# Kernel tuning notes

Measured on AMD Instinct MI355X. Metric: run time of the kernel, lower is better.

## Reference

```python
import jax, jax.numpy as jnp
import numpy as np

NUM_NODES = 50000
NUM_EDGES = 800000
IN_CH = 128
HID = 128
NUM_LAYERS = 3
CONF_HID = 64
TAU0 = 1.0


def _glorot(key, shape):
    lim = (6.0 / (shape[0] + shape[1])) ** 0.5
    return jax.random.uniform(key, shape, jnp.float32, -lim, lim)


def setup_inputs() -> dict:
    key = jax.random.key(0)
    ks = jax.random.split(key, 16)
    inp = {
        "x": jax.random.normal(ks[0], (NUM_NODES, IN_CH), jnp.float32),
        "edge_index": jax.random.randint(ks[1], (2, NUM_EDGES), 0, NUM_NODES, jnp.int32),
    }
    dims = [(IN_CH, HID)] + [(HID, HID)] * (NUM_LAYERS - 1)
    for i, (di, do) in enumerate(dims):
        inp[f"conv_w{i}"] = _glorot(ks[2 + i], (di, do))
        inp[f"conv_b{i}"] = jnp.zeros((do,), jnp.float32)
    inp["conf_w1"] = _glorot(ks[8], (HID, CONF_HID))
    inp["conf_b1"] = jnp.zeros((CONF_HID,), jnp.float32)
    inp["conf_w2"] = _glorot(ks[9], (CONF_HID, 2))
    inp["conf_b2"] = jnp.zeros((2,), jnp.float32)
    inp["temp_w"] = _glorot(ks[10], (HID, 1))
    return inp


def _gcn_conv(x, W, b, src, dst):
    # PyG GCNConv: linear -> add self loops -> sym-normalized aggregate -> bias
    h = x @ W
    loop = jnp.arange(NUM_NODES, dtype=src.dtype)
    s = jnp.concatenate([src, loop])
    d = jnp.concatenate([dst, loop])
    deg = jax.ops.segment_sum(jnp.ones(d.shape, h.dtype), d, num_segments=NUM_NODES)
    dinv = jnp.where(deg > 0, deg ** -0.5, 0.0)
    norm = dinv[s] * dinv[d]  # [E+N]
    out = jax.ops.segment_sum(h[s] * norm[:, None], d, num_segments=NUM_NODES)
    return out + b


def _forward(x, edge_index, conv_ws, conv_bs, conf_w1, conf_b1, conf_w2, conf_b2, temp_w):
    src, dst = edge_index[0], edge_index[1]
    gkey = jax.random.key(42)
    z = jnp.zeros((NUM_NODES, HID), jnp.float32)
    continue_mask = jnp.ones((NUM_NODES,), bool)
    exit_layers = jnp.full((NUM_NODES,), NUM_LAYERS, jnp.int32)
    active = []
    for layer_idx in range(NUM_LAYERS):
        x = _gcn_conv(x, conv_ws[layer_idx], conv_bs[layer_idx], src, dst)
        if layer_idx < NUM_LAYERS - 1:
            x = jax.nn.gelu(x, approximate=False)  # eval mode: dropout is identity
        active.append(jnp.sum(continue_mask).astype(jnp.int32))
        logits = jax.nn.relu(x @ conf_w1 + conf_b1) @ conf_w2 + conf_b2  # [N,2]
        temp = 1.0 / (jax.nn.softplus(x @ temp_w) + TAU0)  # [N,1], always finite
        u = jax.random.uniform(jax.random.fold_in(gkey, layer_idx), logits.shape,
                               jnp.float32, 1e-10, 1.0)
        gumbels = -jnp.log(-jnp.log(u))
        y = jax.nn.softmax((logits + gumbels) / temp, axis=-1)
        exit_decision = y[:, 1] > y[:, 0]
        newly_exited = exit_decision & continue_mask
        z = z + x * newly_exited[:, None].astype(x.dtype)
        exit_layers = jnp.where(newly_exited, layer_idx, exit_layers)
        continue_mask = continue_mask & ~exit_decision
    z = z + x * continue_mask[:, None].astype(x.dtype)
    return z, exit_layers, jnp.stack(active)


def reference(x, edge_index, conv_w0, conv_b0, conv_w1, conv_b1, conv_w2, conv_b2,
              conf_w1, conf_b1, conf_w2, conf_b2, temp_w):
    return _forward(x, edge_index,
                    [conv_w0, conv_w1, conv_w2], [conv_b0, conv_b1, conv_b2],
                    conf_w1, conf_b1, conf_w2, conf_b2, temp_w)
```

## Files before the change

### kernel.cpp

```cpp
#include <hip/hip_runtime.h>
#include <stdint.h>

#define NN 50000
#define NE 800000
#define CH 128

typedef double d4 __attribute__((ext_vector_type(4)));

__host__ __device__ inline void tf2x32(uint32_t k0, uint32_t k1, uint32_t& x0, uint32_t& x1) {
  uint32_t ks2 = k0 ^ k1 ^ 0x1BD11BDAu;
  x0 += k0; x1 += k1;
#define ROTL(v, r) (((v) << (r)) | ((v) >> (32 - (r))))
#define RND(r) { x0 += x1; x1 = ROTL(x1, r); x1 ^= x0; }
  RND(13) RND(15) RND(26) RND(6)
  x0 += k1; x1 += ks2 + 1u;
  RND(17) RND(29) RND(16) RND(24)
  x0 += ks2; x1 += k0 + 2u;
  RND(13) RND(15) RND(26) RND(6)
  x0 += k0; x1 += k1 + 3u;
  RND(17) RND(29) RND(16) RND(24)
  x0 += k1; x1 += ks2 + 4u;
  RND(13) RND(15) RND(26) RND(6)
  x0 += ks2; x1 += k0 + 5u;
#undef RND
#undef ROTL
}

__device__ inline float bits_to_u(uint32_t b) {
  float f = __uint_as_float(0x3F800000u | (b >> 9)) - 1.0f;
  f = f + 1e-10f;
  return fmaxf(1e-10f, f);
}

__global__ __launch_bounds__(256) void deg_k(const int* __restrict__ dst, int* __restrict__ degi) {
  int i = blockIdx.x * 256 + threadIdx.x;
  if (i < NE) atomicAdd(&degi[dst[i]], 1);
}

__global__ __launch_bounds__(256) void dinv_k(const int* __restrict__ degi, float* __restrict__ dinv) {
  int n = blockIdx.x * 256 + threadIdx.x;
  if (n < NN) {
    float d = (float)(degi[n] + 1);
    dinv[n] = 1.0f / sqrtf(d);
  }
}

__global__ __launch_bounds__(256) void scan1_k(const int* __restrict__ degi, int* __restrict__ offs,
                                               int* __restrict__ part) {
  __shared__ int tmp[256];
  int t = threadIdx.x, b = blockIdx.x, i = b * 256 + t;
  int v = (i < NN) ? degi[i] : 0;
  tmp[t] = v;
  __syncthreads();
  for (int s = 1; s < 256; s <<= 1) {
    int a = (t >= s) ? tmp[t - s] : 0;
    __syncthreads();
    tmp[t] += a;
    __syncthreads();
  }
  int incl = tmp[t];
  if (i < NN) offs[i] = incl - v;
  if (t == 255) part[b] = incl;
}

__global__ void scan2_k(int* part, int nparts) {
  if (threadIdx.x == 0 && blockIdx.x == 0) {
    int run = 0;
    for (int i = 0; i < nparts; ++i) { int v = part[i]; part[i] = run; run += v; }
  }
}

__global__ __launch_bounds__(256) void scan3_k(int* __restrict__ offs, const int* __restrict__ part) {
  int i = blockIdx.x * 256 + threadIdx.x;
  if (i < NN) offs[i] += part[blockIdx.x];
  if (i == 0) offs[NN] = NE;
}

__global__ __launch_bounds__(256) void place_k(const int* __restrict__ dst, const int* __restrict__ offs,
                                               int* __restrict__ cnt, int* __restrict__ eids) {
  int i = blockIdx.x * 256 + threadIdx.x;
  if (i < NE) {
    int d = dst[i];
    int p = offs[d] + atomicAdd(&cnt[d], 1);
    eids[p] = i;
  }
}

__global__ __launch_bounds__(256) void sort_k(const int* __restrict__ offs, int* __restrict__ eids) {
  int n = blockIdx.x * 256 + threadIdx.x;
  if (n >= NN) return;
  int s0 = offs[n], s1 = offs[n + 1];
  for (int i = s0 + 1; i < s1; ++i) {
    int v = eids[i];
    int j = i - 1;
    while (j >= s0 && eids[j] > v) { eids[j + 1] = eids[j]; --j; }
    eids[j + 1] = v;
  }
}

__global__ __launch_bounds__(256) void gath_k(const int* __restrict__ eids, const int* __restrict__ src,
                                              const int* __restrict__ dst, const float* __restrict__ dinv,
                                              int* __restrict__ srcs, float* __restrict__ norms) {
  int p = blockIdx.x * 256 + threadIdx.x;
  if (p < NE) {
    int e = eids[p];
    int s = src[e];
    float nm = dinv[s] * dinv[dst[e]];
    srcs[p] = s;
    norms[p] = nm;
  }
}

__global__ __launch_bounds__(256) void gum_k(float* __restrict__ gum,
                                             uint32_t k00, uint32_t k01, uint32_t k10, uint32_t k11,
                                             uint32_t k20, uint32_t k21) {
  int i = blockIdx.x * 256 + threadIdx.x;
  if (i >= 3 * NN) return;
  int l = i / NN;
  int n = i - l * NN;
  uint32_t kx, ky;
  if (l == 0) { kx = k00; ky = k01; }
  else if (l == 1) { kx = k10; ky = k11; }
  else { kx = k20; ky = k21; }
  int j0 = 2 * n, j1 = 2 * n + 1;
  uint32_t w0, w1;
  if (j0 < NN) {
    uint32_t a0 = (uint32_t)j0, a1 = (uint32_t)(j0 + NN);
    tf2x32(kx, ky, a0, a1); w0 = a0;
    uint32_t b0 = (uint32_t)j1, b1 = (uint32_t)(j1 + NN);
    tf2x32(kx, ky, b0, b1); w1 = b0;
  } else {
    uint32_t a0 = (uint32_t)(j0 - NN), a1 = (uint32_t)j0;
    tf2x32(kx, ky, a0, a1); w0 = a1;
    uint32_t b0 = (uint32_t)(j1 - NN), b1 = (uint32_t)j1;
    tf2x32(kx, ky, b0, b1); w1 = b1;
  }
  float u0 = bits_to_u(w0), u1 = bits_to_u(w1);
  gum[2 * (size_t)i]     = -logf(-logf(u0));
  gum[2 * (size_t)i + 1] = -logf(-logf(u1));
}

__global__ __launch_bounds__(256) void einit_k(float* __restrict__ eout) {
  int i = blockIdx.x * 256 + threadIdx.x;
  if (i < NN) eout[i] = 3.0f;
}

__global__ __launch_bounds__(256) void lin_k(const float* __restrict__ x, const float* __restrict__ W,
                                             float* __restrict__ h) {
  __shared__ float Ws[32 * 128];
  __shared__ float xs[64][36];
  int t = threadIdx.x;
  int row0 = blockIdx.x << 6;
  int tr = t & 15, tc = t >> 4;
  float4 acc[4][2];
#pragma unroll
  for (int i = 0; i < 4; ++i) { acc[i][0] = make_float4(0,0,0,0); acc[i][1] = make_float4(0,0,0,0); }

  for (int kt = 0; kt < 4; ++kt) {
    __syncthreads();
    {
      const float4* W4 = (const float4*)(W + (size_t)(kt * 32) * 128);
      float4* Ws4 = (float4*)Ws;
#pragma unroll
      for (int i = 0; i < 4; ++i) Ws4[t + 256 * i] = W4[t + 256 * i];
    }
    {
#pragma unroll
      for (int i = 0; i < 2; ++i) {
        int f = t + 256 * i;
        int row = f >> 3, c4 = f & 7;
        int gr = row0 + row;
        float4 v = make_float4(0,0,0,0);
        if (gr < NN) v = ((const float4*)x)[(size_t)gr * 32 + kt * 8 + c4];
        *(float4*)&xs[row][4 * c4] = v;
      }
    }
    __syncthreads();
    const float4* Ws4 = (const float4*)Ws;
#pragma unroll
    for (int kk = 0; kk < 32; kk += 4) {
      float4 xv[4];
#pragma unroll
      for (int i = 0; i < 4; ++i) xv[i] = *(const float4*)&xs[tr + 16 * i][kk];
#pragma unroll
      for (int d = 0; d < 4; ++d) {
        float4 w0 = Ws4[(kk + d) * 32 + tc];
        float4 w1 = Ws4[(kk + d) * 32 + 16 + tc];
#pragma unroll
        for (int i = 0; i < 4; ++i) {
          float xd = ((const float*)&xv[i])[d];
          acc[i][0].x += xd * w0.x; acc[i][0].y += xd * w0.y;
          acc[i][0].z += xd * w0.z; acc[i][0].w += xd * w0.w;
          acc[i][1].x += xd * w1.x; acc[i][1].y += xd * w1.y;
          acc[i][1].z += xd * w1.z; acc[i][1].w += xd * w1.w;
        }
      }
    }
  }
#pragma unroll
  for (int i = 0; i < 4; ++i) {
    int gr = row0 + tr + 16 * i;
    if (gr < NN) {
      ((float4*)h)[(size_t)gr * 32 + tc] = acc[i][0];
      ((float4*)h)[(size_t)gr * 32 + 16 + tc] = acc[i][1];
    }
  }
}

__device__ inline float gelu_exact(float v) {
  return 0.5f * v * (1.0f + erff(v / 1.4142135623730951f));
}

__global__ __launch_bounds__(256) void agg_k(const float* __restrict__ h, const float* __restrict__ dinv,
                                             const int* __restrict__ offs, const int* __restrict__ srcs,
                                             const float* __restrict__ norms, const float* __restrict__ bias,
                                             float* __restrict__ xout, int act) {
  int lane = threadIdx.x & 63, w = threadIdx.x >> 6;
  int n = blockIdx.x * 4 + w;
  if (n >= NN) return;
  int s0 = offs[n], s1 = offs[n + 1];
  double a0 = 0.0, a1 = 0.0;
  for (int p0 = s0; p0 < s1; p0 += 64) {
    int m = s1 - p0; if (m > 64) m = 64;
    int sv = 0; float nv = 0.f;
    if (lane < m) {
      sv = __builtin_nontemporal_load(&srcs[p0 + lane]);
      nv = __builtin_nontemporal_load(&norms[p0 + lane]);
    }
    int i = 0;
    for (; i + 8 <= m; i += 8) {
      int   sA = __shfl(sv, i),     sB = __shfl(sv, i + 1), sC = __shfl(sv, i + 2), sD = __shfl(sv, i + 3);
      int   sE = __shfl(sv, i + 4), sF = __shfl(sv, i + 5), sG = __shfl(sv, i + 6), sH = __shfl(sv, i + 7);
      float nA = __shfl(nv, i),     nB = __shfl(nv, i + 1), nC = __shfl(nv, i + 2), nD = __shfl(nv, i + 3);
      float nE = __shfl(nv, i + 4), nF = __shfl(nv, i + 5), nG = __shfl(nv, i + 6), nH = __shfl(nv, i + 7);
      float2 hA = *(const float2*)&h[(size_t)sA * CH + 2 * lane];
      float2 hB = *(const float2*)&h[(size_t)sB * CH + 2 * lane];
      float2 hC = *(const float2*)&h[(size_t)sC * CH + 2 * lane];
      float2 hD = *(const float2*)&h[(size_t)sD * CH + 2 * lane];
      float2 hE = *(const float2*)&h[(size_t)sE * CH + 2 * lane];
      float2 hF = *(const float2*)&h[(size_t)sF * CH + 2 * lane];
      float2 hG = *(const float2*)&h[(size_t)sG * CH + 2 * lane];
      float2 hH = *(const float2*)&h[(size_t)sH * CH + 2 * lane];
      a0 += (double)(hA.x * nA); a1 += (double)(hA.y * nA);
      a0 += (double)(hB.x * nB); a1 += (double)(hB.y * nB);
      a0 += (double)(hC.x * nC); a1 += (double)(hC.y * nC);
      a0 += (double)(hD.x * nD); a1 += (double)(hD.y * nD);
      a0 += (double)(hE.x * nE); a1 += (double)(hE.y * nE);
      a0 += (double)(hF.x * nF); a1 += (double)(hF.y * nF);
      a0 += (double)(hG.x * nG); a1 += (double)(hG.y * nG);
      a0 += (double)(hH.x * nH); a1 += (double)(hH.y * nH);
    }
    for (; i + 4 <= m; i += 4) {
      int   sA = __shfl(sv, i),     sB = __shfl(sv, i + 1), sC = __shfl(sv, i + 2), sD = __shfl(sv, i + 3);
      float nA = __shfl(nv, i),     nB = __shfl(nv, i + 1), nC = __shfl(nv, i + 2), nD = __shfl(nv, i + 3);
      float2 hA = *(const float2*)&h[(size_t)sA * CH + 2 * lane];
      float2 hB = *(const float2*)&h[(size_t)sB * CH + 2 * lane];
      float2 hC = *(const float2*)&h[(size_t)sC * CH + 2 * lane];
      float2 hD = *(const float2*)&h[(size_t)sD * CH + 2 * lane];
      a0 += (double)(hA.x * nA); a1 += (double)(hA.y * nA);
      a0 += (double)(hB.x * nB); a1 += (double)(hB.y * nB);
      a0 += (double)(hC.x * nC); a1 += (double)(hC.y * nC);
      a0 += (double)(hD.x * nD); a1 += (double)(hD.y * nD);
    }
    for (; i < m; ++i) {
      int   s = __shfl(sv, i);
      float nm = __shfl(nv, i);
      float2 hv = *(const float2*)&h[(size_t)s * CH + 2 * lane];
      a0 += (double)(hv.x * nm); a1 += (double)(hv.y * nm);
    }
  }
  float dv = dinv[n];
  float selfn = dv * dv;
  float2 hn = *(const float2*)&h[(size_t)n * CH + 2 * lane];
  a0 += (double)(hn.x * selfn); a1 += (double)(hn.y * selfn);
  float r0 = (float)a0 + bias[2 * lane];
  float r1 = (float)a1 + bias[2 * lane + 1];
  if (act) { r0 = gelu_exact(r0); r1 = gelu_exact(r1); }
  float2 o; o.x = r0; o.y = r1;
  *(float2*)&xout[(size_t)n * CH + 2 * lane] = o;
}

template <int MODE>
__global__ __launch_bounds__(256) void decide_k(const float* __restrict__ x, const float* __restrict__ W1,
                                                const float* __restrict__ b1, const float* __restrict__ W2,
                                                const float* __restrict__ b2, const float* __restrict__ gum,
                                                float* __restrict__ zout, float* __restrict__ eout,
                                                float layerf) {
  __shared__ float b1s[64];
  __shared__ float w2s[128];
  __shared__ float b2s[2];
  __shared__ float xs[4][16][132];
  int t = threadIdx.x;
  if (t < 64) b1s[t] = b1[t];
  if (t < 128) w2s[t] = W2[t];
  if (t < 2) b2s[t] = b2[t];

  int lane = t & 63, w = t >> 6;
  int n0 = blockIdx.x * 64 + w * 16;
#pragma unroll
  for (int i = 0; i < 8; ++i) {
    int f = lane + 64 * i;
    int row = f >> 5, c4 = f & 31;
    int gr = n0 + row;
    float4 v = make_float4(0.f, 0.f, 0.f, 0.f);
    if (gr < NN) v = ((const float4*)x)[(size_t)gr * 32 + c4];
    *(float4*)&xs[w][row][4 * c4] = v;
  }

  int g = lane >> 4, r = lane & 15;
  bool writer = (r < 4);
  int mynode = n0 + 4 * g + r;
  float ev = 3.0f;
  float gg0 = 0.f, gg1 = 0.f;
  if (writer && mynode < NN) {
    if (MODE > 0) ev = eout[mynode];
    gg0 = gum[2 * (size_t)mynode];
    gg1 = gum[2 * (size_t)mynode + 1];
  }
  bool m_act = writer && (mynode < NN) && (MODE == 0 || ev == 3.0f);
  unsigned long long actmask = __ballot(m_act);
  __syncthreads();
  if (MODE > 0 && actmask == 0ULL) return;

  d4 acc0 = {0., 0., 0., 0.}, acc1 = {0., 0., 0., 0.};
  d4 acc2 = {0., 0., 0., 0.}, acc3 = {0., 0., 0., 0.};
#pragma unroll 4
  for (int ks = 0; ks < 32; ++ks) {
    int k = 4 * ks + g;
    double av = (double)xs[w][r][k];
    const float* Wk = W1 + (size_t)k * 64;
    double b0 = (double)Wk[r];
    double b1v = (double)Wk[16 + r];
    double b2v = (double)Wk[32 + r];
    double b3v = (double)Wk[48 + r];
    acc0 = __builtin_amdgcn_mfma_f64_16x16x4f64(av, b0, acc0, 0, 0, 0);
    acc1 = __builtin_amdgcn_mfma_f64_16x16x4f64(av, b1v, acc1, 0, 0, 0);
    acc2 = __builtin_amdgcn_mfma_f64_16x16x4f64(av, b2v, acc2, 0, 0, 0);
    acc3 = __builtin_amdgcn_mfma_f64_16x16x4f64(av, b3v, acc3, 0, 0, 0);
  }

  double p0[4], p1[4];
#pragma unroll
  for (int i = 0; i < 4; ++i) {
    float h0 = fmaxf((float)acc0[i] + b1s[r], 0.f);
    float h1 = fmaxf((float)acc1[i] + b1s[16 + r], 0.f);
    float h2 = fmaxf((float)acc2[i] + b1s[32 + r], 0.f);
    float h3 = fmaxf((float)acc3[i] + b1s[48 + r], 0.f);
    double q0 = (double)h0 * (double)w2s[2 * r] + (double)h1 * (double)w2s[2 * (16 + r)] +
                (double)h2 * (double)w2s[2 * (32 + r)] + (double)h3 * (double)w2s[2 * (48 + r)];
    double q1 = (double)h0 * (double)w2s[2 * r + 1] + (double)h1 * (double)w2s[2 * (16 + r) + 1] +
                (double)h2 * (double)w2s[2 * (32 + r) + 1] + (double)h3 * (double)w2s[2 * (48 + r) + 1];
#pragma unroll
    for (int off = 1; off <= 8; off <<= 1) {
      q0 += __shfl_xor(q0, off);
      q1 += __shfl_xor(q1, off);
    }
    p0[i] = q0; p1[i] = q1;
  }

  double q0sel = p0[0], q1sel = p1[0];
  if (r == 1) { q0sel = p0[1]; q1sel = p1[1]; }
  if (r == 2) { q0sel = p0[2]; q1sel = p1[2]; }
  if (r == 3) { q0sel = p0[3]; q1sel = p1[3]; }
  bool myex = false;
  if (writer && mynode < NN) {
    float l0 = (float)q0sel + b2s[0];
    float l1 = (float)q1sel + b2s[1];
    myex = (l1 + gg1) > (l0 + gg0);
  }
  unsigned long long exmask = __ballot(myex);

  if (m_act && myex) eout[mynode] = layerf;

#pragma unroll
  for (int i = 0; i < 16; ++i) {
    int bitpos = 16 * (i >> 2) + (i & 3);
    bool a = (actmask >> bitpos) & 1ULL;
    bool ee = (exmask >> bitpos) & 1ULL;
    if (a && (MODE == 2 || ee)) {
      int node = n0 + i;
      float2 v;
      v.x = xs[w][i][2 * lane];
      v.y = xs[w][i][2 * lane + 1];
      *(float2*)&zout[(size_t)node * CH + 2 * lane] = v;
    }
  }
}

__global__ __launch_bounds__(1024) void cnt_k(const float* __restrict__ eout, float* __restrict__ aout) {
  __shared__ int s1[16], s2[16];
  int t = threadIdx.x;
  int c1 = 0, c2 = 0;
  for (int i = t; i < NN; i += 1024) {
    float v = eout[i];
    c1 += (v < 0.5f);
    c2 += (v < 1.5f);
  }
#pragma unroll
  for (int off = 32; off >= 1; off >>= 1) { c1 += __shfl_xor(c1, off); c2 += __shfl_xor(c2, off); }
  if ((t & 63) == 0) { s1[t >> 6] = c1; s2[t >> 6] = c2; }
  __syncthreads();
  if (t == 0) {
    int a1 = 0, a2 = 0;
#pragma unroll
    for (int i = 0; i < 16; ++i) { a1 += s1[i]; a2 += s2[i]; }
    aout[0] = 50000.0f;
    aout[1] = (float)(NN - a1);
    aout[2] = (float)(NN - a2);
  }
}

extern "C" void kernel_launch(void* const* d_in, const int* in_sizes, int n_in,
                              void* d_out, int out_size, void* d_ws, size_t ws_size,
                              hipStream_t stream) {
  const float* x_in = (const float*)d_in[0];
  const int* eidx = (const int*)d_in[1];
  const int* esrc = eidx;
  const int* edst = eidx + NE;
  const float* convw[3] = {(const float*)d_in[2], (const float*)d_in[4], (const float*)d_in[6]};
  const float* convb[3] = {(const float*)d_in[3], (const float*)d_in[5], (const float*)d_in[7]};
  const float* cw1 = (const float*)d_in[8];
  const float* cb1 = (const float*)d_in[9];
  const float* cw2 = (const float*)d_in[10];
  const float* cb2 = (const float*)d_in[11];

  float* out = (float*)d_out;
  float* zout = out;
  float* eout = out + (size_t)NN * CH;
  float* aout = eout + NN;

  char* w = (char*)d_ws;
  float* P = (float*)w;   w += (size_t)NN * CH * 4;
  float* Q = (float*)w;   w += (size_t)NN * CH * 4;
  int* eids = (int*)w;    w += (size_t)NE * 4;
  float* norms = (float*)w; w += (size_t)NE * 4;
  float* gum = (float*)w; w += (size_t)3 * NN * 2 * 4;
  int* offs = (int*)w;    w += (size_t)(NN + 1) * 4;
  float* dinv = (float*)w; w += (size_t)NN * 4;
  char* zr0 = w;
  int* degi = (int*)w;    w += (size_t)NN * 4;
  int* cnt = (int*)w;     w += (size_t)NN * 4;
  int* parts = (int*)w;   w += 1024;

  hipMemsetAsync(zr0, 0, (size_t)(2 * NN) * 4, stream);

  uint32_t key[3][2];
  for (int l = 0; l < 3; ++l) {
    uint32_t a = 0u, b = (uint32_t)l;
    tf2x32(0u, 42u, a, b);
    key[l][0] = a; key[l][1] = b;
  }

  const int nblkN = (NN + 255) / 256;
  deg_k<<<(NE + 255) / 256, 256, 0, stream>>>(edst, degi);
  dinv_k<<<nblkN, 256, 0, stream>>>(degi, dinv);
  scan1_k<<<nblkN, 256, 0, stream>>>(degi, offs, parts);
  scan2_k<<<1, 64, 0, stream>>>(parts, nblkN);
  scan3_k<<<nblkN, 256, 0, stream>>>(offs, parts);
  place_k<<<(NE + 255) / 256, 256, 0, stream>>>(edst, offs, cnt, eids);
  sort_k<<<nblkN, 256, 0, stream>>>(offs, eids);
  gath_k<<<(NE + 255) / 256, 256, 0, stream>>>(eids, esrc, edst, dinv, eids, norms);
  gum_k<<<(3 * NN + 255) / 256, 256, 0, stream>>>(gum, key[0][0], key[0][1], key[1][0], key[1][1],
                                                  key[2][0], key[2][1]);
  einit_k<<<nblkN, 256, 0, stream>>>(eout);

  const int LB = (NN + 63) / 64;
  const int AB = (NN + 3) / 4;
  const int DB = (NN + 63) / 64;
  for (int l = 0; l < 3; ++l) {
    const float* xin = (l == 0) ? x_in : Q;
    lin_k<<<LB, 256, 0, stream>>>(xin, convw[l], P);
    agg_k<<<AB, 256, 0, stream>>>(P, dinv, offs, eids, norms, convb[l], Q, (l < 2) ? 1 : 0);
    if (l == 0)
      decide_k<0><<<DB, 256, 0, stream>>>(Q, cw1, cb1, cw2, cb2, gum, zout, eout, 0.0f);
    else if (l == 1)
      decide_k<1><<<DB, 256, 0, stream>>>(Q, cw1, cb1, cw2, cb2, gum + (size_t)NN * 2, zout, eout, 1.0f);
    else
      decide_k<2><<<DB, 256, 0, stream>>>(Q, cw1, cb1, cw2, cb2, gum + (size_t)2 * NN * 2, zout, eout, 2.0f);
  }
  cnt_k<<<1, 1024, 0, stream>>>(eout, aout);
}
```

Measured before the change: 526.9 us.

## Fuse exit-decision MLP into next layer's linear kernel and widen aggregation loads

```diff
diff --git a/kernel.cpp b/kernel.cpp
--- a/kernel.cpp
+++ b/kernel.cpp
@@ -37,16 +37,8 @@
   if (i < NE) atomicAdd(&degi[dst[i]], 1);
 }
 
-__global__ __launch_bounds__(256) void dinv_k(const int* __restrict__ degi, float* __restrict__ dinv) {
-  int n = blockIdx.x * 256 + threadIdx.x;
-  if (n < NN) {
-    float d = (float)(degi[n] + 1);
-    dinv[n] = 1.0f / sqrtf(d);
-  }
-}
-
 __global__ __launch_bounds__(256) void scan1_k(const int* __restrict__ degi, int* __restrict__ offs,
-                                               int* __restrict__ part) {
+                                               int* __restrict__ part, float* __restrict__ dinv) {
   __shared__ int tmp[256];
   int t = threadIdx.x, b = blockIdx.x, i = b * 256 + t;
   int v = (i < NN) ? degi[i] : 0;
@@ -59,7 +51,10 @@
     __syncthreads();
   }
   int incl = tmp[t];
-  if (i < NN) offs[i] = incl - v;
+  if (i < NN) {
+    offs[i] = incl - v;
+    dinv[i] = 1.0f / sqrtf((float)(v + 1));
+  }
   if (t == 255) part[b] = incl;
 }
 
@@ -140,18 +135,45 @@
   gum[2 * (size_t)i + 1] = -logf(-logf(u1));
 }
 
-__global__ __launch_bounds__(256) void einit_k(float* __restrict__ eout) {
-  int i = blockIdx.x * 256 + threadIdx.x;
-  if (i < NN) eout[i] = 3.0f;
-}
-
-__global__ __launch_bounds__(256) void lin_k(const float* __restrict__ x, const float* __restrict__ W,
-                                             float* __restrict__ h) {
+template <int DEC>
+__global__ __launch_bounds__(256) void lin_k(const float* __restrict__ xin, const float* __restrict__ W,
+                                             float* __restrict__ h, const float* __restrict__ W1,
+                                             const float* __restrict__ b1, const float* __restrict__ W2,
+                                             const float* __restrict__ b2, const float* __restrict__ gum,
+                                             float* __restrict__ zout, float* __restrict__ eout) {
   __shared__ float Ws[32 * 128];
   __shared__ float xs[64][36];
+  __shared__ float w2s[128];
+  __shared__ float b1s[64];
+  __shared__ float b2s[2];
   int t = threadIdx.x;
   int row0 = blockIdx.x << 6;
   int tr = t & 15, tc = t >> 4;
+
+  int lane = t & 63, w = t >> 6;
+  int g = lane >> 4, r = lane & 15;
+  int n0 = row0 + w * 16;
+  bool writer = (r < 4);
+  int mynode = n0 + 4 * g + r;
+  float ev = 3.0f, gg0 = 0.f, gg1 = 0.f;
+  unsigned long long actmask = 0ULL;
+  bool doMLP = false;
+  d4 acc0 = {0., 0., 0., 0.}, acc1 = {0., 0., 0., 0.};
+  d4 acc2 = {0., 0., 0., 0.}, acc3 = {0., 0., 0., 0.};
+  if (DEC >= 0) {
+    if (t < 64) b1s[t] = b1[t];
+    if (t < 128) w2s[t] = W2[t];
+    if (t < 2) b2s[t] = b2[t];
+    if (writer && mynode < NN) {
+      if (DEC == 1) ev = eout[mynode];
+      gg0 = gum[2 * (size_t)mynode];
+      gg1 = gum[2 * (size_t)mynode + 1];
+    }
+    bool m_act = writer && (mynode < NN) && (DEC == 0 || ev == 3.0f);
+    actmask = __ballot(m_act);
+    doMLP = (DEC == 0) || (actmask != 0ULL);
+  }
+
   float4 acc[4][2];
 #pragma unroll
   for (int i = 0; i < 4; ++i) { acc[i][0] = make_float4(0,0,0,0); acc[i][1] = make_float4(0,0,0,0); }
@@ -171,7 +193,7 @@
         int row = f >> 3, c4 = f & 7;
         int gr = row0 + row;
         float4 v = make_float4(0,0,0,0);
-        if (gr < NN) v = ((const float4*)x)[(size_t)gr * 32 + kt * 8 + c4];
+        if (gr < NN) v = ((const float4*)xin)[(size_t)gr * 32 + kt * 8 + c4];
         *(float4*)&xs[row][4 * c4] = v;
       }
     }
@@ -196,6 +218,23 @@
         }
       }
     }
+    if (DEC >= 0 && doMLP) {
+#pragma unroll
+      for (int ksl = 0; ksl < 8; ++ksl) {
+        int kl = 4 * ksl + g;
+        int kglob = kt * 32 + kl;
+        double av = (double)xs[w * 16 + r][kl];
+        const float* Wk = W1 + (size_t)kglob * 64;
+        double b0v = (double)Wk[r];
+        double b1v = (double)Wk[16 + r];
+        double b2v = (double)Wk[32 + r];
+        double b3v = (double)Wk[48 + r];
+        acc0 = __builtin_amdgcn_mfma_f64_16x16x4f64(av, b0v, acc0, 0, 0, 0);
+        acc1 = __builtin_amdgcn_mfma_f64_16x16x4f64(av, b1v, acc1, 0, 0, 0);
+        acc2 = __builtin_amdgcn_mfma_f64_16x16x4f64(av, b2v, acc2, 0, 0, 0);
+        acc3 = __builtin_amdgcn_mfma_f64_16x16x4f64(av, b3v, acc3, 0, 0, 0);
+      }
+    }
   }
 #pragma unroll
   for (int i = 0; i < 4; ++i) {
@@ -203,6 +242,55 @@
     if (gr < NN) {
       ((float4*)h)[(size_t)gr * 32 + tc] = acc[i][0];
       ((float4*)h)[(size_t)gr * 32 + 16 + tc] = acc[i][1];
+    }
+  }
+
+  if (DEC >= 0 && doMLP) {
+    double p0[4], p1[4];
+#pragma unroll
+    for (int i = 0; i < 4; ++i) {
+      float h0 = fmaxf((float)acc0[i] + b1s[r], 0.f);
+      float h1 = fmaxf((float)acc1[i] + b1s[16 + r], 0.f);
+      float h2 = fmaxf((float)acc2[i] + b1s[32 + r], 0.f);
+      float h3 = fmaxf((float)acc3[i] + b1s[48 + r], 0.f);
+      double q0 = (double)h0 * (double)w2s[2 * r] + (double)h1 * (double)w2s[2 * (16 + r)] +
+                  (double)h2 * (double)w2s[2 * (32 + r)] + (double)h3 * (double)w2s[2 * (48 + r)];
+      double q1 = (double)h0 * (double)w2s[2 * r + 1] + (double)h1 * (double)w2s[2 * (16 + r) + 1] +
+                  (double)h2 * (double)w2s[2 * (32 + r) + 1] + (double)h3 * (double)w2s[2 * (48 + r) + 1];
+#pragma unroll
+      for (int off = 1; off <= 8; off <<= 1) {
+        q0 += __shfl_xor(q0, off);
+        q1 += __shfl_xor(q1, off);
+      }
+      p0[i] = q0; p1[i] = q1;
+    }
+    double q0sel = p0[0], q1sel = p1[0];
+    if (r == 1) { q0sel = p0[1]; q1sel = p1[1]; }
+    if (r == 2) { q0sel = p0[2]; q1sel = p1[2]; }
+    if (r == 3) { q0sel = p0[3]; q1sel = p1[3]; }
+    bool myex = false;
+    if (writer && mynode < NN) {
+      float l0 = (float)q0sel + b2s[0];
+      float l1 = (float)q1sel + b2s[1];
+      myex = (l1 + gg1) > (l0 + gg0);
+    }
+    unsigned long long exmask = __ballot(myex);
+    bool m_act = (actmask >> (16 * g + r)) & 1ULL;
+    if (DEC == 0) {
+      if (writer && mynode < NN) eout[mynode] = myex ? 0.0f : 3.0f;
+    } else {
+      if (m_act && myex) eout[mynode] = 1.0f;
+    }
+#pragma unroll
+    for (int i = 0; i < 16; ++i) {
+      int bitpos = 16 * (i >> 2) + (i & 3);
+      bool a = (actmask >> bitpos) & 1ULL;
+      bool ee = (exmask >> bitpos) & 1ULL;
+      if (a && ee) {
+        int node = n0 + i;
+        float2 v = *(const float2*)&xin[(size_t)node * CH + 2 * lane];
+        *(float2*)&zout[(size_t)node * CH + 2 * lane] = v;
+      }
     }
   }
 }
@@ -218,8 +306,9 @@
   int lane = threadIdx.x & 63, w = threadIdx.x >> 6;
   int n = blockIdx.x * 4 + w;
   if (n >= NN) return;
+  int c4 = lane & 31, hh = lane >> 5;
   int s0 = offs[n], s1 = offs[n + 1];
-  double a0 = 0.0, a1 = 0.0;
+  double a0 = 0.0, a1 = 0.0, a2 = 0.0, a3 = 0.0;
   for (int p0 = s0; p0 < s1; p0 += 64) {
     int m = s1 - p0; if (m > 64) m = 64;
     int sv = 0; float nv = 0.f;
@@ -229,63 +318,49 @@
     }
     int i = 0;
     for (; i + 8 <= m; i += 8) {
-      int   sA = __shfl(sv, i),     sB = __shfl(sv, i + 1), sC = __shfl(sv, i + 2), sD = __shfl(sv, i + 3);
-      int   sE = __shfl(sv, i + 4), sF = __shfl(sv, i + 5), sG = __shfl(sv, i + 6), sH = __shfl(sv, i + 7);
-      float nA = __shfl(nv, i),     nB = __shfl(nv, i + 1), nC = __shfl(nv, i + 2), nD = __shfl(nv, i + 3);
-      float nE = __shfl(nv, i + 4), nF = __shfl(nv, i + 5), nG = __shfl(nv, i + 6), nH = __shfl(nv, i + 7);
-      float2 hA = *(const float2*)&h[(size_t)sA * CH + 2 * lane];
-      float2 hB = *(const float2*)&h[(size_t)sB * CH + 2 * lane];
-      float2 hC = *(const float2*)&h[(size_t)sC * CH + 2 * lane];
-      float2 hD = *(const float2*)&h[(size_t)sD * CH + 2 * lane];
-      float2 hE = *(const float2*)&h[(size_t)sE * CH + 2 * lane];
-      float2 hF = *(const float2*)&h[(size_t)sF * CH + 2 * lane];
-      float2 hG = *(const float2*)&h[(size_t)sG * CH + 2 * lane];
-      float2 hH = *(const float2*)&h[(size_t)sH * CH + 2 * lane];
-      a0 += (double)(hA.x * nA); a1 += (double)(hA.y * nA);
-      a0 += (double)(hB.x * nB); a1 += (double)(hB.y * nB);
-      a0 += (double)(hC.x * nC); a1 += (double)(hC.y * nC);
-      a0 += (double)(hD.x * nD); a1 += (double)(hD.y * nD);
-      a0 += (double)(hE.x * nE); a1 += (double)(hE.y * nE);
-      a0 += (double)(hF.x * nF); a1 += (double)(hF.y * nF);
-      a0 += (double)(hG.x * nG); a1 += (double)(hG.y * nG);
-      a0 += (double)(hH.x * nH); a1 += (double)(hH.y * nH);
-    }
-    for (; i + 4 <= m; i += 4) {
-      int   sA = __shfl(sv, i),     sB = __shfl(sv, i + 1), sC = __shfl(sv, i + 2), sD = __shfl(sv, i + 3);
-      float nA = __shfl(nv, i),     nB = __shfl(nv, i + 1), nC = __shfl(nv, i + 2), nD = __shfl(nv, i + 3);
-      float2 hA = *(const float2*)&h[(size_t)sA * CH + 2 * lane];
-      float2 hB = *(const float2*)&h[(size_t)sB * CH + 2 * lane];
-      float2 hC = *(const float2*)&h[(size_t)sC * CH + 2 * lane];
-      float2 hD = *(const float2*)&h[(size_t)sD * CH + 2 * lane];
-      a0 += (double)(hA.x * nA); a1 += (double)(hA.y * nA);
-      a0 += (double)(hB.x * nB); a1 += (double)(hB.y * nB);
-      a0 += (double)(hC.x * nC); a1 += (double)(hC.y * nC);
-      a0 += (double)(hD.x * nD); a1 += (double)(hD.y * nD);
-    }
-    for (; i < m; ++i) {
-      int   s = __shfl(sv, i);
-      float nm = __shfl(nv, i);
-      float2 hv = *(const float2*)&h[(size_t)s * CH + 2 * lane];
-      a0 += (double)(hv.x * nm); a1 += (double)(hv.y * nm);
-    }
-  }
-  float dv = dinv[n];
-  float selfn = dv * dv;
-  float2 hn = *(const float2*)&h[(size_t)n * CH + 2 * lane];
-  a0 += (double)(hn.x * selfn); a1 += (double)(hn.y * selfn);
-  float r0 = (float)a0 + bias[2 * lane];
-  float r1 = (float)a1 + bias[2 * lane + 1];
-  if (act) { r0 = gelu_exact(r0); r1 = gelu_exact(r1); }
-  float2 o; o.x = r0; o.y = r1;
-  *(float2*)&xout[(size_t)n * CH + 2 * lane] = o;
-}
-
-template <int MODE>
-__global__ __launch_bounds__(256) void decide_k(const float* __restrict__ x, const float* __restrict__ W1,
-                                                const float* __restrict__ b1, const float* __restrict__ W2,
-                                                const float* __restrict__ b2, const float* __restrict__ gum,
-                                                float* __restrict__ zout, float* __restrict__ eout,
-                                                float layerf) {
+      int   sA = __shfl(sv, i + hh),     sB = __shfl(sv, i + 2 + hh);
+      int   sC = __shfl(sv, i + 4 + hh), sD = __shfl(sv, i + 6 + hh);
+      float nA = __shfl(nv, i + hh),     nB = __shfl(nv, i + 2 + hh);
+      float nC = __shfl(nv, i + 4 + hh), nD = __shfl(nv, i + 6 + hh);
+      float4 hA = *(const float4*)&h[(size_t)sA * CH + 4 * c4];
+      float4 hB = *(const float4*)&h[(size_t)sB * CH + 4 * c4];
+      float4 hC = *(const float4*)&h[(size_t)sC * CH + 4 * c4];
+      float4 hD = *(const float4*)&h[(size_t)sD * CH + 4 * c4];
+      a0 += (double)(hA.x * nA); a1 += (double)(hA.y * nA); a2 += (double)(hA.z * nA); a3 += (double)(hA.w * nA);
+      a0 += (double)(hB.x * nB); a1 += (double)(hB.y * nB); a2 += (double)(hB.z * nB); a3 += (double)(hB.w * nB);
+      a0 += (double)(hC.x * nC); a1 += (double)(hC.y * nC); a2 += (double)(hC.z * nC); a3 += (double)(hC.w * nC);
+      a0 += (double)(hD.x * nD); a1 += (double)(hD.y * nD); a2 += (double)(hD.z * nD); a3 += (double)(hD.w * nD);
+    }
+    for (; i < m; i += 2) {
+      int   s = __shfl(sv, i + hh);
+      float nm = __shfl(nv, i + hh);
+      float4 hv = *(const float4*)&h[(size_t)s * CH + 4 * c4];
+      a0 += (double)(hv.x * nm); a1 += (double)(hv.y * nm); a2 += (double)(hv.z * nm); a3 += (double)(hv.w * nm);
+    }
+  }
+  a0 += __shfl_xor(a0, 32); a1 += __shfl_xor(a1, 32);
+  a2 += __shfl_xor(a2, 32); a3 += __shfl_xor(a3, 32);
+  if (hh == 0) {
+    float dv = dinv[n];
+    float selfn = dv * dv;
+    float4 hn = *(const float4*)&h[(size_t)n * CH + 4 * c4];
+    a0 += (double)(hn.x * selfn); a1 += (double)(hn.y * selfn);
+    a2 += (double)(hn.z * selfn); a3 += (double)(hn.w * selfn);
+    float4 bv = *(const float4*)&bias[4 * c4];
+    float r0 = (float)a0 + bv.x;
+    float r1 = (float)a1 + bv.y;
+    float r2 = (float)a2 + bv.z;
+    float r3 = (float)a3 + bv.w;
+    if (act) { r0 = gelu_exact(r0); r1 = gelu_exact(r1); r2 = gelu_exact(r2); r3 = gelu_exact(r3); }
+    float4 o; o.x = r0; o.y = r1; o.z = r2; o.w = r3;
+    *(float4*)&xout[(size_t)n * CH + 4 * c4] = o;
+  }
+}
+
+__global__ __launch_bounds__(256) void decide2_k(const float* __restrict__ x, const float* __restrict__ W1,
+                                                 const float* __restrict__ b1, const float* __restrict__ W2,
+                                                 const float* __restrict__ b2, const float* __restrict__ gum,
+                                                 float* __restrict__ zout, float* __restrict__ eout) {
   __shared__ float b1s[64];
   __shared__ float w2s[128];
   __shared__ float b2s[2];
@@ -310,17 +385,16 @@
   int g = lane >> 4, r = lane & 15;
   bool writer = (r < 4);
   int mynode = n0 + 4 * g + r;
-  float ev = 3.0f;
-  float gg0 = 0.f, gg1 = 0.f;
+  float ev = 3.0f, gg0 = 0.f, gg1 = 0.f;
   if (writer && mynode < NN) {
-    if (MODE > 0) ev = eout[mynode];
+    ev = eout[mynode];
     gg0 = gum[2 * (size_t)mynode];
     gg1 = gum[2 * (size_t)mynode + 1];
   }
-  bool m_act = writer && (mynode < NN) && (MODE == 0 || ev == 3.0f);
+  bool m_act = writer && (mynode < NN) && (ev == 3.0f);
   unsigned long long actmask = __ballot(m_act);
   __syncthreads();
-  if (MODE > 0 && actmask == 0ULL) return;
+  if (actmask == 0ULL) return;
 
   d4 acc0 = {0., 0., 0., 0.}, acc1 = {0., 0., 0., 0.};
   d4 acc2 = {0., 0., 0., 0.}, acc3 = {0., 0., 0., 0.};
@@ -370,14 +444,13 @@
   }
   unsigned long long exmask = __ballot(myex);
 
-  if (m_act && myex) eout[mynode] = layerf;
+  if (m_act && myex) eout[mynode] = 2.0f;
 
 #pragma unroll
   for (int i = 0; i < 16; ++i) {
     int bitpos = 16 * (i >> 2) + (i & 3);
     bool a = (actmask >> bitpos) & 1ULL;
-    bool ee = (exmask >> bitpos) & 1ULL;
-    if (a && (MODE == 2 || ee)) {
+    if (a) {
       int node = n0 + i;
       float2 v;
       v.x = xs[w][i][2 * lane];
@@ -391,10 +464,10 @@
   __shared__ int s1[16], s2[16];
   int t = threadIdx.x;
   int c1 = 0, c2 = 0;
-  for (int i = t; i < NN; i += 1024) {
-    float v = eout[i];
-    c1 += (v < 0.5f);
-    c2 += (v < 1.5f);
+  for (int i = t; i < NN / 4; i += 1024) {
+    float4 v = ((const float4*)eout)[i];
+    c1 += (v.x < 0.5f) + (v.y < 0.5f) + (v.z < 0.5f) + (v.w < 0.5f);
+    c2 += (v.x < 1.5f) + (v.y < 1.5f) + (v.z < 1.5f) + (v.w < 1.5f);
   }
 #pragma unroll
   for (int off = 32; off >= 1; off >>= 1) { c1 += __shfl_xor(c1, off); c2 += __shfl_xor(c2, off); }
@@ -453,8 +526,7 @@
 
   const int nblkN = (NN + 255) / 256;
   deg_k<<<(NE + 255) / 256, 256, 0, stream>>>(edst, degi);
-  dinv_k<<<nblkN, 256, 0, stream>>>(degi, dinv);
-  scan1_k<<<nblkN, 256, 0, stream>>>(degi, offs, parts);
+  scan1_k<<<nblkN, 256, 0, stream>>>(degi, offs, parts, dinv);
   scan2_k<<<1, 64, 0, stream>>>(parts, nblkN);
   scan3_k<<<nblkN, 256, 0, stream>>>(offs, parts);
   place_k<<<(NE + 255) / 256, 256, 0, stream>>>(edst, offs, cnt, eids);
@@ -462,21 +534,16 @@
   gath_k<<<(NE + 255) / 256, 256, 0, stream>>>(eids, esrc, edst, dinv, eids, norms);
   gum_k<<<(3 * NN + 255) / 256, 256, 0, stream>>>(gum, key[0][0], key[0][1], key[1][0], key[1][1],
                                                   key[2][0], key[2][1]);
-  einit_k<<<nblkN, 256, 0, stream>>>(eout);
 
   const int LB = (NN + 63) / 64;
   const int AB = (NN + 3) / 4;
-  const int DB = (NN + 63) / 64;
-  for (int l = 0; l < 3; ++l) {
-    const float* xin = (l == 0) ? x_in : Q;
-    lin_k<<<LB, 256, 0, stream>>>(xin, convw[l], P);
-    agg_k<<<AB, 256, 0, stream>>>(P, dinv, offs, eids, norms, convb[l], Q, (l < 2) ? 1 : 0);
-    if (l == 0)
-      decide_k<0><<<DB, 256, 0, stream>>>(Q, cw1, cb1, cw2, cb2, gum, zout, eout, 0.0f);
-    else if (l == 1)
-      decide_k<1><<<DB, 256, 0, stream>>>(Q, cw1, cb1, cw2, cb2, gum + (size_t)NN * 2, zout, eout, 1.0f);
-    else
-      decide_k<2><<<DB, 256, 0, stream>>>(Q, cw1, cb1, cw2, cb2, gum + (size_t)2 * NN * 2, zout, eout, 2.0f);
-  }
+  lin_k<-1><<<LB, 256, 0, stream>>>(x_in, convw[0], P, nullptr, nullptr, nullptr, nullptr,
+                                    nullptr, nullptr, nullptr);
+  agg_k<<<AB, 256, 0, stream>>>(P, dinv, offs, eids, norms, convb[0], Q, 1);
+  lin_k<0><<<LB, 256, 0, stream>>>(Q, convw[1], P, cw1, cb1, cw2, cb2, gum, zout, eout);
+  agg_k<<<AB, 256, 0, stream>>>(P, dinv, offs, eids, norms, convb[1], Q, 1);
+  lin_k<1><<<LB, 256, 0, stream>>>(Q, convw[2], P, cw1, cb1, cw2, cb2, gum + (size_t)NN * 2, zout, eout);
+  agg_k<<<AB, 256, 0, stream>>>(P, dinv, offs, eids, norms, convb[2], Q, 0);
+  decide2_k<<<LB, 256, 0, stream>>>(Q, cw1, cb1, cw2, cb2, gum + (size_t)2 * NN * 2, zout, eout);
   cnt_k<<<1, 1024, 0, stream>>>(eout, aout);
 }
```

Measured after the change: 563.6 us. 7.0% more time.

## Drop CSR sort, fuse gather into placement, widen aggregation to float4 half-waves

Applied to the files above, without the earlier changes.

```diff
diff --git a/kernel.cpp b/kernel.cpp
--- a/kernel.cpp
+++ b/kernel.cpp
@@ -37,16 +37,8 @@
   if (i < NE) atomicAdd(&degi[dst[i]], 1);
 }
 
-__global__ __launch_bounds__(256) void dinv_k(const int* __restrict__ degi, float* __restrict__ dinv) {
-  int n = blockIdx.x * 256 + threadIdx.x;
-  if (n < NN) {
-    float d = (float)(degi[n] + 1);
-    dinv[n] = 1.0f / sqrtf(d);
-  }
-}
-
 __global__ __launch_bounds__(256) void scan1_k(const int* __restrict__ degi, int* __restrict__ offs,
-                                               int* __restrict__ part) {
+                                               int* __restrict__ part, float* __restrict__ dinv) {
   __shared__ int tmp[256];
   int t = threadIdx.x, b = blockIdx.x, i = b * 256 + t;
   int v = (i < NN) ? degi[i] : 0;
@@ -59,7 +51,10 @@
     __syncthreads();
   }
   int incl = tmp[t];
-  if (i < NN) offs[i] = incl - v;
+  if (i < NN) {
+    offs[i] = incl - v;
+    dinv[i] = 1.0f / sqrtf((float)(v + 1));
+  }
   if (t == 255) part[b] = incl;
 }
 
@@ -76,38 +71,16 @@
   if (i == 0) offs[NN] = NE;
 }
 
-__global__ __launch_bounds__(256) void place_k(const int* __restrict__ dst, const int* __restrict__ offs,
-                                               int* __restrict__ cnt, int* __restrict__ eids) {
+__global__ __launch_bounds__(256) void place_k(const int* __restrict__ src, const int* __restrict__ dst,
+                                               const int* __restrict__ offs, const float* __restrict__ dinv,
+                                               int* __restrict__ cnt, int* __restrict__ srcs,
+                                               float* __restrict__ norms) {
   int i = blockIdx.x * 256 + threadIdx.x;
   if (i < NE) {
-    int d = dst[i];
+    int d = dst[i], s = src[i];
     int p = offs[d] + atomicAdd(&cnt[d], 1);
-    eids[p] = i;
-  }
-}
-
-__global__ __launch_bounds__(256) void sort_k(const int* __restrict__ offs, int* __restrict__ eids) {
-  int n = blockIdx.x * 256 + threadIdx.x;
-  if (n >= NN) return;
-  int s0 = offs[n], s1 = offs[n + 1];
-  for (int i = s0 + 1; i < s1; ++i) {
-    int v = eids[i];
-    int j = i - 1;
-    while (j >= s0 && eids[j] > v) { eids[j + 1] = eids[j]; --j; }
-    eids[j + 1] = v;
-  }
-}
-
-__global__ __launch_bounds__(256) void gath_k(const int* __restrict__ eids, const int* __restrict__ src,
-                                              const int* __restrict__ dst, const float* __restrict__ dinv,
-                                              int* __restrict__ srcs, float* __restrict__ norms) {
-  int p = blockIdx.x * 256 + threadIdx.x;
-  if (p < NE) {
-    int e = eids[p];
-    int s = src[e];
-    float nm = dinv[s] * dinv[dst[e]];
     srcs[p] = s;
-    norms[p] = nm;
+    norms[p] = dinv[s] * dinv[d];
   }
 }
 
@@ -218,8 +191,9 @@
   int lane = threadIdx.x & 63, w = threadIdx.x >> 6;
   int n = blockIdx.x * 4 + w;
   if (n >= NN) return;
+  int c4 = lane & 31, hh = lane >> 5;
   int s0 = offs[n], s1 = offs[n + 1];
-  double a0 = 0.0, a1 = 0.0;
+  double a0 = 0.0, a1 = 0.0, a2 = 0.0, a3 = 0.0;
   for (int p0 = s0; p0 < s1; p0 += 64) {
     int m = s1 - p0; if (m > 64) m = 64;
     int sv = 0; float nv = 0.f;
@@ -229,55 +203,43 @@
     }
     int i = 0;
     for (; i + 8 <= m; i += 8) {
-      int   sA = __shfl(sv, i),     sB = __shfl(sv, i + 1), sC = __shfl(sv, i + 2), sD = __shfl(sv, i + 3);
-      int   sE = __shfl(sv, i + 4), sF = __shfl(sv, i + 5), sG = __shfl(sv, i + 6), sH = __shfl(sv, i + 7);
-      float nA = __shfl(nv, i),     nB = __shfl(nv, i + 1), nC = __shfl(nv, i + 2), nD = __shfl(nv, i + 3);
-      float nE = __shfl(nv, i + 4), nF = __shfl(nv, i + 5), nG = __shfl(nv, i + 6), nH = __shfl(nv, i + 7);
-      float2 hA = *(const float2*)&h[(size_t)sA * CH + 2 * lane];
-      float2 hB = *(const float2*)&h[(size_t)sB * CH + 2 * lane];
-      float2 hC = *(const float2*)&h[(size_t)sC * CH + 2 * lane];
-      float2 hD = *(const float2*)&h[(size_t)sD * CH + 2 * lane];
-      float2 hE = *(const float2*)&h[(size_t)sE * CH + 2 * lane];
-      float2 hF = *(const float2*)&h[(size_t)sF * CH + 2 * lane];
-      float2 hG = *(const float2*)&h[(size_t)sG * CH + 2 * lane];
-      float2 hH = *(const float2*)&h[(size_t)sH * CH + 2 * lane];
-      a0 += (double)(hA.x * nA); a1 += (double)(hA.y * nA);
-      a0 += (double)(hB.x * nB); a1 += (double)(hB.y * nB);
-      a0 += (double)(hC.x * nC); a1 += (double)(hC.y * nC);
-      a0 += (double)(hD.x * nD); a1 += (double)(hD.y * nD);
-      a0 += (double)(hE.x * nE); a1 += (double)(hE.y * nE);
-      a0 += (double)(hF.x * nF); a1 += (double)(hF.y * nF);
-      a0 += (double)(hG.x * nG); a1 += (double)(hG.y * nG);
-      a0 += (double)(hH.x * nH); a1 += (double)(hH.y * nH);
-    }
-    for (; i + 4 <= m; i += 4) {
-      int   sA = __shfl(sv, i),     sB = __shfl(sv, i + 1), sC = __shfl(sv, i + 2), sD = __shfl(sv, i + 3);
-      float nA = __shfl(nv, i),     nB = __shfl(nv, i + 1), nC = __shfl(nv, i + 2), nD = __shfl(nv, i + 3);
-      float2 hA = *(const float2*)&h[(size_t)sA * CH + 2 * lane];
-      float2 hB = *(const float2*)&h[(size_t)sB * CH + 2 * lane];
-      float2 hC = *(const float2*)&h[(size_t)sC * CH + 2 * lane];
-      float2 hD = *(const float2*)&h[(size_t)sD * CH + 2 * lane];
-      a0 += (double)(hA.x * nA); a1 += (double)(hA.y * nA);
-      a0 += (double)(hB.x * nB); a1 += (double)(hB.y * nB);
-      a0 += (double)(hC.x * nC); a1 += (double)(hC.y * nC);
-      a0 += (double)(hD.x * nD); a1 += (double)(hD.y * nD);
-    }
-    for (; i < m; ++i) {
-      int   s = __shfl(sv, i);
-      float nm = __shfl(nv, i);
-      float2 hv = *(const float2*)&h[(size_t)s * CH + 2 * lane];
-      a0 += (double)(hv.x * nm); a1 += (double)(hv.y * nm);
-    }
-  }
-  float dv = dinv[n];
-  float selfn = dv * dv;
-  float2 hn = *(const float2*)&h[(size_t)n * CH + 2 * lane];
-  a0 += (double)(hn.x * selfn); a1 += (double)(hn.y * selfn);
-  float r0 = (float)a0 + bias[2 * lane];
-  float r1 = (float)a1 + bias[2 * lane + 1];
-  if (act) { r0 = gelu_exact(r0); r1 = gelu_exact(r1); }
-  float2 o; o.x = r0; o.y = r1;
-  *(float2*)&xout[(size_t)n * CH + 2 * lane] = o;
+      int   sA = __shfl(sv, i + hh),     sB = __shfl(sv, i + 2 + hh);
+      int   sC = __shfl(sv, i + 4 + hh), sD = __shfl(sv, i + 6 + hh);
+      float nA = __shfl(nv, i + hh),     nB = __shfl(nv, i + 2 + hh);
+      float nC = __shfl(nv, i + 4 + hh), nD = __shfl(nv, i + 6 + hh);
+      float4 hA = *(const float4*)&h[(size_t)sA * CH + 4 * c4];
+      float4 hB = *(const float4*)&h[(size_t)sB * CH + 4 * c4];
+      float4 hC = *(const float4*)&h[(size_t)sC * CH + 4 * c4];
+      float4 hD = *(const float4*)&h[(size_t)sD * CH + 4 * c4];
+      a0 += (double)(hA.x * nA); a1 += (double)(hA.y * nA); a2 += (double)(hA.z * nA); a3 += (double)(hA.w * nA);
+      a0 += (double)(hB.x * nB); a1 += (double)(hB.y * nB); a2 += (double)(hB.z * nB); a3 += (double)(hB.w * nB);
+      a0 += (double)(hC.x * nC); a1 += (double)(hC.y * nC); a2 += (double)(hC.z * nC); a3 += (double)(hC.w * nC);
+      a0 += (double)(hD.x * nD); a1 += (double)(hD.y * nD); a2 += (double)(hD.z * nD); a3 += (double)(hD.w * nD);
+    }
+    for (; i < m; i += 2) {
+      int   s = __shfl(sv, i + hh);
+      float nm = __shfl(nv, i + hh);
+      float4 hv = *(const float4*)&h[(size_t)s * CH + 4 * c4];
+      a0 += (double)(hv.x * nm); a1 += (double)(hv.y * nm); a2 += (double)(hv.z * nm); a3 += (double)(hv.w * nm);
+    }
+  }
+  a0 += __shfl_xor(a0, 32); a1 += __shfl_xor(a1, 32);
+  a2 += __shfl_xor(a2, 32); a3 += __shfl_xor(a3, 32);
+  if (hh == 0) {
+    float dv = dinv[n];
+    float selfn = dv * dv;
+    float4 hn = *(const float4*)&h[(size_t)n * CH + 4 * c4];
+    a0 += (double)(hn.x * selfn); a1 += (double)(hn.y * selfn);
+    a2 += (double)(hn.z * selfn); a3 += (double)(hn.w * selfn);
+    float4 bv = *(const float4*)&bias[4 * c4];
+    float r0 = (float)a0 + bv.x;
+    float r1 = (float)a1 + bv.y;
+    float r2 = (float)a2 + bv.z;
+    float r3 = (float)a3 + bv.w;
+    if (act) { r0 = gelu_exact(r0); r1 = gelu_exact(r1); r2 = gelu_exact(r2); r3 = gelu_exact(r3); }
+    float4 o; o.x = r0; o.y = r1; o.z = r2; o.w = r3;
+    *(float4*)&xout[(size_t)n * CH + 4 * c4] = o;
+  }
 }
 
 template <int MODE>
@@ -391,10 +353,10 @@
   __shared__ int s1[16], s2[16];
   int t = threadIdx.x;
   int c1 = 0, c2 = 0;
-  for (int i = t; i < NN; i += 1024) {
-    float v = eout[i];
-    c1 += (v < 0.5f);
-    c2 += (v < 1.5f);
+  for (int i = t; i < NN / 4; i += 1024) {
+    float4 v = ((const float4*)eout)[i];
+    c1 += (v.x < 0.5f) + (v.y < 0.5f) + (v.z < 0.5f) + (v.w < 0.5f);
+    c2 += (v.x < 1.5f) + (v.y < 1.5f) + (v.z < 1.5f) + (v.w < 1.5f);
   }
 #pragma unroll
   for (int off = 32; off >= 1; off >>= 1) { c1 += __shfl_xor(c1, off); c2 += __shfl_xor(c2, off); }
@@ -432,7 +394,7 @@
   char* w = (char*)d_ws;
   float* P = (float*)w;   w += (size_t)NN * CH * 4;
   float* Q = (float*)w;   w += (size_t)NN * CH * 4;
-  int* eids = (int*)w;    w += (size_t)NE * 4;
+  int* srcs = (int*)w;    w += (size_t)NE * 4;
   float* norms = (float*)w; w += (size_t)NE * 4;
   float* gum = (float*)w; w += (size_t)3 * NN * 2 * 4;
   int* offs = (int*)w;    w += (size_t)(NN + 1) * 4;
@@ -453,13 +415,10 @@
 
   const int nblkN = (NN + 255) / 256;
   deg_k<<<(NE + 255) / 256, 256, 0, stream>>>(edst, degi);
-  dinv_k<<<nblkN, 256, 0, stream>>>(degi, dinv);
-  scan1_k<<<nblkN, 256, 0, stream>>>(degi, offs, parts);
+  scan1_k<<<nblkN, 256, 0, stream>>>(degi, offs, parts, dinv);
   scan2_k<<<1, 64, 0, stream>>>(parts, nblkN);
   scan3_k<<<nblkN, 256, 0, stream>>>(offs, parts);
-  place_k<<<(NE + 255) / 256, 256, 0, stream>>>(edst, offs, cnt, eids);
-  sort_k<<<nblkN, 256, 0, stream>>>(offs, eids);
-  gath_k<<<(NE + 255) / 256, 256, 0, stream>>>(eids, esrc, edst, dinv, eids, norms);
+  place_k<<<(NE + 255) / 256, 256, 0, stream>>>(esrc, edst, offs, dinv, cnt, srcs, norms);
   gum_k<<<(3 * NN + 255) / 256, 256, 0, stream>>>(gum, key[0][0], key[0][1], key[1][0], key[1][1],
                                                   key[2][0], key[2][1]);
   einit_k<<<nblkN, 256, 0, stream>>>(eout);
@@ -470,7 +429,7 @@
   for (int l = 0; l < 3; ++l) {
     const float* xin = (l == 0) ? x_in : Q;
     lin_k<<<LB, 256, 0, stream>>>(xin, convw[l], P);
-    agg_k<<<AB, 256, 0, stream>>>(P, dinv, offs, eids, norms, convb[l], Q, (l < 2) ? 1 : 0);
+    agg_k<<<AB, 256, 0, stream>>>(P, dinv, offs, srcs, norms, convb[l], Q, (l < 2) ? 1 : 0);
     if (l == 0)
       decide_k<0><<<DB, 256, 0, stream>>>(Q, cw1, cb1, cw2, cb2, gum, zout, eout, 0.0f);
     else if (l == 1)
```

New measurement: 469.2 us. 11.0% less time.
